# Performance work log

Measured on AMD Instinct MI355X. Metric: run time of the kernel, lower is better.

## Reference

```python
import jax, jax.numpy as jnp
import numpy as np
import math

COARSE_K = 20
FINE_K = 10
KNOWLEDGE_RANK = 128


def setup_inputs() -> dict:
    key = jax.random.key(0)
    ks = jax.random.split(key, 5)
    B, S, D = 2, 2048, 1024
    NK = 65536
    return {
        "x": jax.random.normal(ks[0], (B, S, D), dtype=jnp.float32),
        "W_router": jax.random.normal(ks[1], (D, NK), dtype=jnp.float32) * 0.02,
        "W_enc": jax.random.normal(ks[2], (D, KNOWLEDGE_RANK), dtype=jnp.float32) * 0.02,
        "K_all": jax.random.normal(ks[3], (NK, KNOWLEDGE_RANK), dtype=jnp.float32) * 0.02,
        "V_all": jax.random.normal(ks[4], (NK, D), dtype=jnp.float32) * 0.02,
    }


def reference(x, W_router, W_enc, K_all, V_all):
    # Stage 1: coarse routing over full knowledge table
    k_logits = jnp.einsum('bsd,dn->bsn', x, W_router)          # [B,S,NK]
    coarse_scores, candidate_idx = jax.lax.top_k(k_logits, COARSE_K)  # [B,S,Ck]

    # Stage 2: fine scoring against gathered coarse candidates
    query = jnp.einsum('bsd,dr->bsr', x, W_enc)                # [B,S,R]
    K_candidates = K_all[candidate_idx]                        # [B,S,Ck,R]
    fine_scores = jnp.einsum('bsr,bscr->bsc', query, K_candidates) / math.sqrt(KNOWLEDGE_RANK)

    fine_topk_scores, fine_local_idx = jax.lax.top_k(fine_scores, FINE_K)  # [B,S,Fk]
    fine_weights = jax.nn.softmax(fine_topk_scores, axis=-1)
    fine_global_idx = jnp.take_along_axis(candidate_idx, fine_local_idx, axis=-1)  # [B,S,Fk]

    selected_V = V_all[fine_global_idx]                        # [B,S,Fk,D]
    output = jnp.einsum('bsfd,bsf->bsd', selected_V, fine_weights)
    return output
```

## Files before the change

### kernel.cpp

```cpp
#include <hip/hip_runtime.h>

#define DIM 1024
#define NKN 65536
#define TOK 4096
#define CK 20
#define FK 10
#define RNK 128
#define CAP 256
#define NCHUNK 512

typedef __bf16 v8bf __attribute__((ext_vector_type(8)));
typedef float v4f __attribute__((ext_vector_type(4)));

#define AS1 __attribute__((address_space(1)))
#define AS3 __attribute__((address_space(3)))

__device__ __forceinline__ unsigned short f2bf(float f) {
  unsigned u = __builtin_bit_cast(unsigned, f);
  u += 0x7FFFu + ((u >> 16) & 1u);
  return (unsigned short)(u >> 16);
}
__device__ __forceinline__ unsigned short bf2key(unsigned short b) {
  return (b & 0x8000) ? (unsigned short)(~b) : (unsigned short)(b | 0x8000);
}

__global__ __launch_bounds__(256) void k_transpose(const float* __restrict__ W,
                                                   float* __restrict__ WT,
                                                   unsigned short* __restrict__ WTb) {
  __shared__ float tile[32][33];
  const int n0 = (blockIdx.x & 2047) << 5;
  const int d0 = (blockIdx.x >> 11) << 5;
  const int c = threadIdx.x & 31, r0 = threadIdx.x >> 5;
#pragma unroll
  for (int i = 0; i < 4; i++) {
    int r = r0 + i * 8;
    tile[r][c] = W[(size_t)(d0 + r) * NKN + n0 + c];
  }
  __syncthreads();
#pragma unroll
  for (int i = 0; i < 4; i++) {
    int r = r0 + i * 8;
    float v = tile[c][r];
    size_t o = (size_t)(n0 + r) * DIM + d0 + c;
    WT[o] = v;
    WTb[o] = f2bf(v);
  }
}

__global__ __launch_bounds__(256) void k_cvt_x(const float* __restrict__ x,
                                               unsigned short* __restrict__ xb) {
  const int i = blockIdx.x * 256 + threadIdx.x;
  const float4 v = reinterpret_cast<const float4*>(x)[i];
  ushort4 o;
  o.x = f2bf(v.x); o.y = f2bf(v.y); o.z = f2bf(v.z); o.w = f2bf(v.w);
  reinterpret_cast<ushort4*>(xb)[i] = o;
}

__global__ __launch_bounds__(512, 4) void k_gemm(const unsigned short* __restrict__ A,
                                                 const unsigned short* __restrict__ Bt,
                                                 unsigned short* __restrict__ Lg,
                                                 unsigned short* __restrict__ CmaxT) {
  __shared__ __align__(16) char lds[73728];
  const int tid = threadIdx.x;
  const int lane = tid & 63, wid = tid >> 6;
  const int wm = wid >> 1, wn = wid & 1;
  const int mb = blockIdx.x & 15, nb = blockIdx.x >> 4;
  const int m0 = mb << 8, n0 = nb << 7;
  const int rm = lane & 15, lq = lane >> 4;
  v4f acc[4][4] = {};

  const int u8 = (((tid & 3) ^ ((tid >> 3) & 3)) << 3);
  const unsigned short* aSrc = A + (size_t)(m0 + (tid >> 2)) * DIM + u8;
  const unsigned short* bSrc = Bt + (size_t)(n0 + (tid >> 2)) * DIM + u8;

  const int sx = ((lq ^ ((rm >> 1) & 3)) << 4);
  const int aOff = (wm * 64 + rm) * 64 + sx;
  const int bOff = 16384 + (wn * 64 + rm) * 64 + sx;

#define STAGE(SLOT, KT) do { \
    char* _b = lds + (SLOT) * 24576 + tid * 16; \
    __builtin_amdgcn_global_load_lds((const AS1 void*)(aSrc + (KT)),             (AS3 void*)(_b),         16, 0, 0); \
    __builtin_amdgcn_global_load_lds((const AS1 void*)(aSrc + (KT) + 128 * DIM), (AS3 void*)(_b + 8192),  16, 0, 0); \
    __builtin_amdgcn_global_load_lds((const AS1 void*)(bSrc + (KT)),             (AS3 void*)(_b + 16384), 16, 0, 0); \
  } while (0)

#define TILE(T, VM, DOSTAGE) do { \
    asm volatile("s_waitcnt vmcnt(" VM ")" ::: "memory"); \
    __builtin_amdgcn_s_barrier(); \
    if (DOSTAGE) STAGE(((T) + 2) % 3, ((T) + 2) * 32); \
    const char* sb = lds + ((T) % 3) * 24576; \
    v8bf a0 = *(const v8bf*)(sb + aOff); \
    v8bf a1 = *(const v8bf*)(sb + aOff + 1024); \
    v8bf a2 = *(const v8bf*)(sb + aOff + 2048); \
    v8bf a3 = *(const v8bf*)(sb + aOff + 3072); \
    v8bf b0 = *(const v8bf*)(sb + bOff); \
    v8bf b1 = *(const v8bf*)(sb + bOff + 1024); \
    v8bf b2 = *(const v8bf*)(sb + bOff + 2048); \
    v8bf b3 = *(const v8bf*)(sb + bOff + 3072); \
    __builtin_amdgcn_s_setprio(1); \
    _Pragma("unroll") for (int nf = 0; nf < 4; ++nf) { \
      v8bf bb = (nf == 0) ? b0 : (nf == 1) ? b1 : (nf == 2) ? b2 : b3; \
      acc[0][nf] = __builtin_amdgcn_mfma_f32_16x16x32_bf16(a0, bb, acc[0][nf], 0, 0, 0); \
      acc[1][nf] = __builtin_amdgcn_mfma_f32_16x16x32_bf16(a1, bb, acc[1][nf], 0, 0, 0); \
      acc[2][nf] = __builtin_amdgcn_mfma_f32_16x16x32_bf16(a2, bb, acc[2][nf], 0, 0, 0); \
      acc[3][nf] = __builtin_amdgcn_mfma_f32_16x16x32_bf16(a3, bb, acc[3][nf], 0, 0, 0); \
    } \
    __builtin_amdgcn_s_setprio(0); \
  } while (0)

  STAGE(0, 0);
  STAGE(1, 32);

  for (int t = 0; t < 30; ++t) {
    TILE(t, "3", true);
  }
  TILE(30, "3", false);
  TILE(31, "0", false);
#undef TILE
#undef STAGE

  const int mr = lq * 4;
  float rmax[4][4];
#pragma unroll
  for (int fr = 0; fr < 4; ++fr) {
#pragma unroll
    for (int r = 0; r < 4; ++r) {
      float mx = acc[fr][0][r];
#pragma unroll
      for (int nf = 1; nf < 4; ++nf) mx = fmaxf(mx, acc[fr][nf][r]);
      rmax[fr][r] = mx;
    }
#pragma unroll
    for (int nf = 0; nf < 4; ++nf) {
      const int mrow = m0 + wm * 64 + fr * 16 + mr;
      const int ncol = n0 + wn * 64 + nf * 16 + rm;
#pragma unroll
      for (int r = 0; r < 4; ++r)
        Lg[(size_t)(mrow + r) * NKN + ncol] = f2bf(acc[fr][nf][r]);
    }
  }
#pragma unroll
  for (int fr = 0; fr < 4; ++fr)
#pragma unroll
    for (int r = 0; r < 4; ++r) {
#pragma unroll
      for (int off = 1; off < 16; off <<= 1)
        rmax[fr][r] = fmaxf(rmax[fr][r], __shfl_xor(rmax[fr][r], off));
    }
  __syncthreads();
  float* smax = (float*)lds;
  if (rm == 0) {
#pragma unroll
    for (int fr = 0; fr < 4; ++fr)
#pragma unroll
      for (int r = 0; r < 4; ++r)
        smax[wn * 256 + wm * 64 + fr * 16 + mr + r] = rmax[fr][r];
  }
  __syncthreads();
  if (tid < 256) {
    float v = fmaxf(smax[tid], smax[256 + tid]);
    CmaxT[(size_t)nb * TOK + m0 + tid] = bf2key(f2bf(v));
  }
}

__global__ __launch_bounds__(256) void k_pickscore(const unsigned short* __restrict__ CmaxT,
                                                   const unsigned short* __restrict__ Lg,
                                                   const float* __restrict__ x,
                                                   const float* __restrict__ WT,
                                                   int* __restrict__ coarse) {
  __shared__ unsigned short keys[NCHUNK];
  __shared__ int qlist[NCHUNK];
  __shared__ float xs[DIM];
  __shared__ double sc[CAP];
  __shared__ int ci[CAP];
  __shared__ int qn, scnt, bsS;
  const int t = blockIdx.x, tid = threadIdx.x;
  const int lane = tid & 63, w = tid >> 6;
  keys[tid] = CmaxT[(size_t)tid * TOK + t];
  keys[tid + 256] = CmaxT[(size_t)(tid + 256) * TOK + t];
  for (int i = tid; i < DIM; i += 256) xs[i] = x[(size_t)t * DIM + i];
  if (tid == 0) { qn = 0; scnt = 0; }
  __syncthreads();
  if (w == 0) {
    int v[8];
#pragma unroll
    for (int j = 0; j < 8; j++) v[j] = keys[lane * 8 + j];
    int t32 = 0;
    for (int it = 0; it < 32; it++) {
      int lm = v[0];
#pragma unroll
      for (int j = 1; j < 8; j++) lm = max(lm, v[j]);
      int gm = lm;
#pragma unroll
      for (int off = 32; off > 0; off >>= 1) gm = max(gm, __shfl_xor(gm, off));
      unsigned long long msk = __ballot(lm == gm);
      if (lane == __ffsll((long long)msk) - 1) {
        bool done = false;
#pragma unroll
        for (int j = 0; j < 8; j++)
          if (!done && v[j] == gm) { v[j] = -1; done = true; }
      }
      t32 = gm;
    }
    if (lane == 0) bsS = t32;
  }
  __syncthreads();
  const int bs = bsS;
  for (int c = tid; c < NCHUNK; c += 256)
    if ((int)keys[c] >= bs) { int p = atomicAdd(&qn, 1); qlist[p] = c; }
  __syncthreads();
  const int nq = qn;
  const int sub = tid >> 7, e = tid & 127;
  for (int qi = sub; qi < nq; qi += 2) {
    const int col = qlist[qi] * 128 + e;
    unsigned short key = bf2key(Lg[(size_t)t * NKN + col]);
    if ((int)key >= bs) {
      int p = atomicAdd(&scnt, 1);
      if (p < CAP) ci[p] = col;
    }
  }
  __syncthreads();
  const int cnt = min(scnt, CAP);
  for (int i = tid; i < CAP; i += 256)
    if (i >= cnt) ci[i] = 0;
  for (int i = tid; i < CAP; i += 256) sc[i] = -1e300;
  __syncthreads();
  for (int c = w; c < cnt; c += 4) {
    const float* wr = WT + (size_t)ci[c] * DIM;
    double sacc = 0.0;
#pragma unroll 4
    for (int i = lane; i < DIM; i += 64) sacc += (double)xs[i] * (double)wr[i];
#pragma unroll
    for (int off = 32; off > 0; off >>= 1) sacc += __shfl_down(sacc, off);
    if (lane == 0) sc[c] = sacc;
  }
  __syncthreads();
  if (w == 0) {
    double v[4];
    int ix[4];
#pragma unroll
    for (int j = 0; j < 4; j++) { v[j] = sc[lane + j * 64]; ix[j] = lane + j * 64; }
    for (int kk = 0; kk < CK; kk++) {
      double v1 = v[0]; int i1 = ix[0];
#pragma unroll
      for (int j = 1; j < 4; j++)
        if (v[j] > v1) { v1 = v[j]; i1 = ix[j]; }
#pragma unroll
      for (int off = 32; off > 0; off >>= 1) {
        double ov = __shfl_down(v1, off);
        int oi = __shfl_down(i1, off);
        if (ov > v1) { v1 = ov; i1 = oi; }
      }
      i1 = __shfl(i1, 0);
      if (lane == 0) coarse[(size_t)t * CK + kk] = ci[i1];
#pragma unroll
      for (int j = 0; j < 4; j++)
        if (i1 == ix[j]) v[j] = -1e300;
    }
  }
}

__global__ __launch_bounds__(256) void k_fine(const float* __restrict__ x,
                                              const float* __restrict__ Wenc,
                                              const float* __restrict__ Kall,
                                              const float* __restrict__ Vall,
                                              const int* __restrict__ coarse,
                                              float* __restrict__ out) {
  __shared__ float xs[DIM];
  __shared__ float pq[2][RNK];
  __shared__ float qs[RNK];
  __shared__ float fsc[CK];
  __shared__ int gix[CK];
  __shared__ float wts[FK];
  __shared__ int fidx[FK];
  const int t = blockIdx.x, tid = threadIdx.x;
  const int lane = tid & 63, w = tid >> 6;
  reinterpret_cast<float4*>(xs)[tid] = reinterpret_cast<const float4*>(x + (size_t)t * DIM)[tid];
  if (tid < CK) gix[tid] = coarse[(size_t)t * CK + tid];
  __syncthreads();
  {
    const int j = tid & 127, half = tid >> 7;
    float s = 0.f;
    const int d0 = half * 512;
#pragma unroll 8
    for (int d = 0; d < 512; d++)
      s = fmaf(xs[d0 + d], Wenc[(size_t)(d0 + d) * RNK + j], s);
    pq[half][j] = s;
  }
  __syncthreads();
  if (tid < RNK) qs[tid] = pq[0][tid] + pq[1][tid];
  __syncthreads();
  for (int c = w; c < CK; c += 4) {
    const float* kr = Kall + (size_t)gix[c] * RNK;
    float s = 0.f;
    s = fmaf(qs[lane], kr[lane], s);
    s = fmaf(qs[lane + 64], kr[lane + 64], s);
#pragma unroll
    for (int off = 32; off > 0; off >>= 1) s += __shfl_down(s, off);
    if (lane == 0) fsc[c] = s * 0.08838834764831843f;
  }
  __syncthreads();
  if (w == 0) {
    float vv = (lane < CK) ? fsc[lane] : -3e38f;
    float myv = -3e38f; int myp = 0;
    for (int kk = 0; kk < FK; kk++) {
      float v1 = vv; int p1 = lane;
#pragma unroll
      for (int off = 32; off > 0; off >>= 1) {
        float ov = __shfl_down(v1, off);
        int op = __shfl_down(p1, off);
        if (ov > v1) { v1 = ov; p1 = op; }
      }
      v1 = __shfl(v1, 0); p1 = __shfl(p1, 0);
      if (lane == kk) { myv = v1; myp = p1; }
      if (lane == p1) vv = -3e38f;
    }
    float sv = (lane < FK) ? myv : -3e38f;
    float mx = sv;
#pragma unroll
    for (int off = 8; off > 0; off >>= 1) mx = fmaxf(mx, __shfl_xor(mx, off, 16));
    float e = (lane < FK) ? expf(sv - mx) : 0.f;
    float se = e;
#pragma unroll
    for (int off = 8; off > 0; off >>= 1) se += __shfl_xor(se, off, 16);
    if (lane < FK) { wts[lane] = e / se; fidx[lane] = gix[myp]; }
  }
  __syncthreads();
  float4 a = make_float4(0.f, 0.f, 0.f, 0.f);
#pragma unroll
  for (int f = 0; f < FK; f++) {
    const float wt = wts[f];
    const float4 v = *reinterpret_cast<const float4*>(&Vall[(size_t)fidx[f] * DIM + tid * 4]);
    a.x = fmaf(wt, v.x, a.x);
    a.y = fmaf(wt, v.y, a.y);
    a.z = fmaf(wt, v.z, a.z);
    a.w = fmaf(wt, v.w, a.w);
  }
  *reinterpret_cast<float4*>(&out[(size_t)t * DIM + tid * 4]) = a;
}


extern "C" void kernel_launch(void* const* d_in, const int* in_sizes, int n_in,
                              void* d_out, int out_size, void* d_ws, size_t ws_size,
                              hipStream_t stream) {
  const float* x = (const float*)d_in[0];
  const float* Wr = (const float*)d_in[1];
  const float* Wenc = (const float*)d_in[2];
  const float* Kall = (const float*)d_in[3];
  const float* Vall = (const float*)d_in[4];
  float* out = (float*)d_out;

  char* ws = (char*)d_ws;
  constexpr size_t OFF_WT = 0;
  constexpr size_t OFF_WTB = 268435456;
  constexpr size_t OFF_XB = 402653184;
  constexpr size_t OFF_LG = 411041792;
  constexpr size_t OFF_CMAX = 947912704;
  float* WT = (float*)(ws + OFF_WT);
  unsigned short* WTb = (unsigned short*)(ws + OFF_WTB);
  unsigned short* xb = (unsigned short*)(ws + OFF_XB);
  unsigned short* Lg = (unsigned short*)(ws + OFF_LG);
  unsigned short* CmaxT = (unsigned short*)(ws + OFF_CMAX);
  int* coarse = (int*)(ws + OFF_XB);

  k_transpose<<<65536, 256, 0, stream>>>(Wr, WT, WTb);
  k_cvt_x<<<4096, 256, 0, stream>>>(x, xb);
  k_gemm<<<8192, 512, 0, stream>>>(xb, WTb, Lg, CmaxT);
  k_pickscore<<<4096, 256, 0, stream>>>(CmaxT, Lg, x, WT, coarse);
  k_fine<<<4096, 256, 0, stream>>>(x, Wenc, Kall, Vall, coarse, out);
}
```

Baseline: 1.048 ms.

## Batch eight tokens per block in fine stage and widen pickscore blocks

k_fine now handles eight tokens per block, so each Wenc element it loads feeds eight query accumulators instead of one. This cuts the per-token reload of the 512KB Wenc matrix across 4096 blocks. k_pickscore moves to 512 threads with float4 loads for x and the rescoring dot products. The trade-off is fewer k_fine blocks (512), which lowers parallelism and raises register and LDS use per block.

```diff
diff --git a/kernel.cpp b/kernel.cpp
--- a/kernel.cpp
+++ b/kernel.cpp
@@ -163,22 +163,23 @@
   }
 }
 
-__global__ __launch_bounds__(256) void k_pickscore(const unsigned short* __restrict__ CmaxT,
+__global__ __launch_bounds__(512) void k_pickscore(const unsigned short* __restrict__ CmaxT,
                                                    const unsigned short* __restrict__ Lg,
                                                    const float* __restrict__ x,
                                                    const float* __restrict__ WT,
                                                    int* __restrict__ coarse) {
   __shared__ unsigned short keys[NCHUNK];
   __shared__ int qlist[NCHUNK];
-  __shared__ float xs[DIM];
+  __shared__ __align__(16) float xs[DIM];
   __shared__ double sc[CAP];
   __shared__ int ci[CAP];
   __shared__ int qn, scnt, bsS;
   const int t = blockIdx.x, tid = threadIdx.x;
   const int lane = tid & 63, w = tid >> 6;
   keys[tid] = CmaxT[(size_t)tid * TOK + t];
-  keys[tid + 256] = CmaxT[(size_t)(tid + 256) * TOK + t];
-  for (int i = tid; i < DIM; i += 256) xs[i] = x[(size_t)t * DIM + i];
+  if (tid < 256)
+    reinterpret_cast<float4*>(xs)[tid] =
+        reinterpret_cast<const float4*>(x + (size_t)t * DIM)[tid];
   if (tid == 0) { qn = 0; scnt = 0; }
   __syncthreads();
   if (w == 0) {
@@ -206,12 +207,11 @@
   }
   __syncthreads();
   const int bs = bsS;
-  for (int c = tid; c < NCHUNK; c += 256)
-    if ((int)keys[c] >= bs) { int p = atomicAdd(&qn, 1); qlist[p] = c; }
+  if ((int)keys[tid] >= bs) { int p = atomicAdd(&qn, 1); qlist[p] = tid; }
   __syncthreads();
   const int nq = qn;
   const int sub = tid >> 7, e = tid & 127;
-  for (int qi = sub; qi < nq; qi += 2) {
+  for (int qi = sub; qi < nq; qi += 4) {
     const int col = qlist[qi] * 128 + e;
     unsigned short key = bf2key(Lg[(size_t)t * NKN + col]);
     if ((int)key >= bs) {
@@ -221,15 +221,22 @@
   }
   __syncthreads();
   const int cnt = min(scnt, CAP);
-  for (int i = tid; i < CAP; i += 256)
+  for (int i = tid; i < CAP; i += 512) {
     if (i >= cnt) ci[i] = 0;
-  for (int i = tid; i < CAP; i += 256) sc[i] = -1e300;
-  __syncthreads();
-  for (int c = w; c < cnt; c += 4) {
-    const float* wr = WT + (size_t)ci[c] * DIM;
+    sc[i] = -1e300;
+  }
+  __syncthreads();
+  for (int c = w; c < cnt; c += 8) {
+    const float4* wr = reinterpret_cast<const float4*>(WT + (size_t)ci[c] * DIM);
+    const float4* xv4 = reinterpret_cast<const float4*>(xs);
     double sacc = 0.0;
-#pragma unroll 4
-    for (int i = lane; i < DIM; i += 64) sacc += (double)xs[i] * (double)wr[i];
+#pragma unroll
+    for (int k = 0; k < 4; k++) {
+      float4 wv = wr[k * 64 + lane];
+      float4 xv = xv4[k * 64 + lane];
+      sacc += (double)xv.x * wv.x + (double)xv.y * wv.y
+            + (double)xv.z * wv.z + (double)xv.w * wv.w;
+    }
 #pragma unroll
     for (int off = 32; off > 0; off >>= 1) sacc += __shfl_down(sacc, off);
     if (lane == 0) sc[c] = sacc;
@@ -266,42 +273,66 @@
                                               const float* __restrict__ Vall,
                                               const int* __restrict__ coarse,
                                               float* __restrict__ out) {
-  __shared__ float xs[DIM];
-  __shared__ float pq[2][RNK];
-  __shared__ float qs[RNK];
-  __shared__ float fsc[CK];
-  __shared__ int gix[CK];
-  __shared__ float wts[FK];
-  __shared__ int fidx[FK];
-  const int t = blockIdx.x, tid = threadIdx.x;
+  __shared__ __align__(16) float xs8[8][DIM];
+  __shared__ float pq[2][8][RNK];
+  __shared__ float q8[8][RNK];
+  __shared__ float fsc8[8][CK];
+  __shared__ int gix8[8][CK];
+  __shared__ float wts8[8][FK];
+  __shared__ int fidx8[8][FK];
+  const int t0 = blockIdx.x * 8, tid = threadIdx.x;
   const int lane = tid & 63, w = tid >> 6;
-  reinterpret_cast<float4*>(xs)[tid] = reinterpret_cast<const float4*>(x + (size_t)t * DIM)[tid];
-  if (tid < CK) gix[tid] = coarse[(size_t)t * CK + tid];
+  for (int i = tid; i < 2048; i += 256)
+    reinterpret_cast<float4*>(&xs8[0][0])[i] =
+        reinterpret_cast<const float4*>(x + (size_t)t0 * DIM)[i];
+  for (int i = tid; i < 8 * CK; i += 256)
+    gix8[i / CK][i % CK] = coarse[(size_t)(t0 + i / CK) * CK + i % CK];
   __syncthreads();
   {
-    const int j = tid & 127, half = tid >> 7;
-    float s = 0.f;
-    const int d0 = half * 512;
-#pragma unroll 8
-    for (int d = 0; d < 512; d++)
-      s = fmaf(xs[d0 + d], Wenc[(size_t)(d0 + d) * RNK + j], s);
-    pq[half][j] = s;
-  }
-  __syncthreads();
-  if (tid < RNK) qs[tid] = pq[0][tid] + pq[1][tid];
-  __syncthreads();
-  for (int c = w; c < CK; c += 4) {
-    const float* kr = Kall + (size_t)gix[c] * RNK;
-    float s = 0.f;
-    s = fmaf(qs[lane], kr[lane], s);
-    s = fmaf(qs[lane + 64], kr[lane + 64], s);
-#pragma unroll
-    for (int off = 32; off > 0; off >>= 1) s += __shfl_down(s, off);
-    if (lane == 0) fsc[c] = s * 0.08838834764831843f;
-  }
-  __syncthreads();
-  if (w == 0) {
-    float vv = (lane < CK) ? fsc[lane] : -3e38f;
+    const int j = tid & 127, g = tid >> 7;
+    float s[8] = {0.f, 0.f, 0.f, 0.f, 0.f, 0.f, 0.f, 0.f};
+    const float4* xv4 = reinterpret_cast<const float4*>(&xs8[0][0]);
+    for (int dc = g * 128; dc < g * 128 + 128; dc++) {
+      float4 xv[8];
+#pragma unroll
+      for (int tok = 0; tok < 8; tok++) xv[tok] = xv4[tok * 256 + dc];
+      const int d = dc * 4;
+      const float w0v = Wenc[(size_t)d * RNK + j];
+      const float w1v = Wenc[(size_t)(d + 1) * RNK + j];
+      const float w2v = Wenc[(size_t)(d + 2) * RNK + j];
+      const float w3v = Wenc[(size_t)(d + 3) * RNK + j];
+#pragma unroll
+      for (int tok = 0; tok < 8; tok++) {
+        s[tok] = fmaf(xv[tok].x, w0v, s[tok]);
+        s[tok] = fmaf(xv[tok].y, w1v, s[tok]);
+        s[tok] = fmaf(xv[tok].z, w2v, s[tok]);
+        s[tok] = fmaf(xv[tok].w, w3v, s[tok]);
+      }
+    }
+#pragma unroll
+    for (int tok = 0; tok < 8; tok++) pq[g][tok][j] = s[tok];
+  }
+  __syncthreads();
+  for (int i = tid; i < 8 * RNK; i += 256)
+    q8[i >> 7][i & 127] = pq[0][i >> 7][i & 127] + pq[1][i >> 7][i & 127];
+  __syncthreads();
+#pragma unroll
+  for (int tt = 0; tt < 2; tt++) {
+    const int tok = w + tt * 4;
+    for (int c = 0; c < CK; c++) {
+      const float* kr = Kall + (size_t)gix8[tok][c] * RNK;
+      float s = fmaf(q8[tok][lane], kr[lane], 0.f);
+      s = fmaf(q8[tok][lane + 64], kr[lane + 64], s);
+#pragma unroll
+      for (int off = 32; off > 0; off >>= 1) s += __shfl_down(s, off);
+      if (lane == 0) fsc8[tok][c] = s * 0.08838834764831843f;
+    }
+  }
+  __syncthreads();
+#pragma unroll
+  for (int tt = 0; tt < 2; tt++) {
+    const int tok = w + tt * 4;
+    float vv = (lane < CK) ? fsc8[tok][lane] : -3e38f;
     float myv = -3e38f; int myp = 0;
     for (int kk = 0; kk < FK; kk++) {
       float v1 = vv; int p1 = lane;
@@ -323,20 +354,23 @@
     float se = e;
 #pragma unroll
     for (int off = 8; off > 0; off >>= 1) se += __shfl_xor(se, off, 16);
-    if (lane < FK) { wts[lane] = e / se; fidx[lane] = gix[myp]; }
-  }
-  __syncthreads();
-  float4 a = make_float4(0.f, 0.f, 0.f, 0.f);
-#pragma unroll
-  for (int f = 0; f < FK; f++) {
-    const float wt = wts[f];
-    const float4 v = *reinterpret_cast<const float4*>(&Vall[(size_t)fidx[f] * DIM + tid * 4]);
-    a.x = fmaf(wt, v.x, a.x);
-    a.y = fmaf(wt, v.y, a.y);
-    a.z = fmaf(wt, v.z, a.z);
-    a.w = fmaf(wt, v.w, a.w);
-  }
-  *reinterpret_cast<float4*>(&out[(size_t)t * DIM + tid * 4]) = a;
+    if (lane < FK) { wts8[tok][lane] = e / se; fidx8[tok][lane] = gix8[tok][myp]; }
+  }
+  __syncthreads();
+  for (int tok = 0; tok < 8; tok++) {
+    float4 a = make_float4(0.f, 0.f, 0.f, 0.f);
+#pragma unroll
+    for (int f = 0; f < FK; f++) {
+      const float wt = wts8[tok][f];
+      const float4 v = *reinterpret_cast<const float4*>(
+          &Vall[(size_t)fidx8[tok][f] * DIM + tid * 4]);
+      a.x = fmaf(wt, v.x, a.x);
+      a.y = fmaf(wt, v.y, a.y);
+      a.z = fmaf(wt, v.z, a.z);
+      a.w = fmaf(wt, v.w, a.w);
+    }
+    *reinterpret_cast<float4*>(&out[(size_t)(t0 + tok) * DIM + tid * 4]) = a;
+  }
 }
 
 
@@ -366,6 +400,6 @@
   k_transpose<<<65536, 256, 0, stream>>>(Wr, WT, WTb);
   k_cvt_x<<<4096, 256, 0, stream>>>(x, xb);
   k_gemm<<<8192, 512, 0, stream>>>(xb, WTb, Lg, CmaxT);
-  k_pickscore<<<4096, 256, 0, stream>>>(CmaxT, Lg, x, WT, coarse);
-  k_fine<<<4096, 256, 0, stream>>>(x, Wenc, Kall, Vall, coarse, out);
-}
+  k_pickscore<<<4096, 512, 0, stream>>>(CmaxT, Lg, x, WT, coarse);
+  k_fine<<<512, 256, 0, stream>>>(x, Wenc, Kall, Vall, coarse, out);
+}
```

Result: slower. 1.104 ms (+5.3%).

## Emit per-chunk top-8 candidates from GEMM epilogue instead of full logits

Applied to the files above, without the earlier changes.

The GEMM epilogue stages bf16 sort keys for its 256x128 tile in LDS. Each row then keeps a sorted top-8 list of packed (key<<16 | column) values and writes only those eight words per row and chunk. This replaces the full bf16 logit matrix and the chunk-max array. The pickscore kernel reads these compact lists, derives the threshold from each chunk's best entry, and collects candidates directly without re-reading logits. The fp64 rescoring dot product also moves to float4 loads. This removes a very large global write and the later gather, at the cost of a serial insertion sort in the epilogue. It assumes no chunk holds more than eight of a row's threshold-passing entries.

```diff
diff --git a/kernel.cpp b/kernel.cpp
--- a/kernel.cpp
+++ b/kernel.cpp
@@ -58,8 +58,7 @@
 
 __global__ __launch_bounds__(512, 4) void k_gemm(const unsigned short* __restrict__ A,
                                                  const unsigned short* __restrict__ Bt,
-                                                 unsigned short* __restrict__ Lg,
-                                                 unsigned short* __restrict__ CmaxT) {
+                                                 unsigned* __restrict__ Ttop) {
   __shared__ __align__(16) char lds[73728];
   const int tid = threadIdx.x;
   const int lane = tid & 63, wid = tid >> 6;
@@ -119,72 +118,79 @@
 #undef TILE
 #undef STAGE
 
-  const int mr = lq * 4;
-  float rmax[4][4];
+  __syncthreads();
+  unsigned short* keys = (unsigned short*)lds;
 #pragma unroll
   for (int fr = 0; fr < 4; ++fr) {
-#pragma unroll
-    for (int r = 0; r < 4; ++r) {
-      float mx = acc[fr][0][r];
-#pragma unroll
-      for (int nf = 1; nf < 4; ++nf) mx = fmaxf(mx, acc[fr][nf][r]);
-      rmax[fr][r] = mx;
-    }
+    const int lrow = wm * 64 + fr * 16 + lq * 4;
 #pragma unroll
     for (int nf = 0; nf < 4; ++nf) {
-      const int mrow = m0 + wm * 64 + fr * 16 + mr;
-      const int ncol = n0 + wn * 64 + nf * 16 + rm;
+      const int lcol = wn * 64 + nf * 16 + rm;
 #pragma unroll
       for (int r = 0; r < 4; ++r)
-        Lg[(size_t)(mrow + r) * NKN + ncol] = f2bf(acc[fr][nf][r]);
-    }
-  }
-#pragma unroll
-  for (int fr = 0; fr < 4; ++fr)
-#pragma unroll
-    for (int r = 0; r < 4; ++r) {
-#pragma unroll
-      for (int off = 1; off < 16; off <<= 1)
-        rmax[fr][r] = fmaxf(rmax[fr][r], __shfl_xor(rmax[fr][r], off));
-    }
-  __syncthreads();
-  float* smax = (float*)lds;
-  if (rm == 0) {
-#pragma unroll
-    for (int fr = 0; fr < 4; ++fr)
-#pragma unroll
-      for (int r = 0; r < 4; ++r)
-        smax[wn * 256 + wm * 64 + fr * 16 + mr + r] = rmax[fr][r];
+        keys[(lrow + r) * 136 + lcol] = bf2key(f2bf(acc[fr][nf][r]));
+    }
   }
   __syncthreads();
   if (tid < 256) {
-    float v = fmaxf(smax[tid], smax[256 + tid]);
-    CmaxT[(size_t)nb * TOK + m0 + tid] = bf2key(f2bf(v));
-  }
-}
-
-__global__ __launch_bounds__(256) void k_pickscore(const unsigned short* __restrict__ CmaxT,
-                                                   const unsigned short* __restrict__ Lg,
+    const uint4* krow = (const uint4*)((const char*)lds + tid * 272);
+    unsigned s0 = 0, s1 = 0, s2 = 0, s3 = 0, s4 = 0, s5 = 0, s6 = 0, s7 = 0;
+#pragma unroll 4
+    for (int k = 0; k < 16; ++k) {
+      const uint4 wv = krow[k];
+      const unsigned base = (unsigned)(n0 + k * 8);
+      const unsigned wd[4] = {wv.x, wv.y, wv.z, wv.w};
+#pragma unroll
+      for (int q = 0; q < 4; ++q) {
+        const unsigned c0 = ((wd[q] & 0xFFFFu) << 16) | (base + 2 * q);
+        const unsigned c1 = (wd[q] & 0xFFFF0000u) | (base + 2 * q + 1);
+#define INS(C) \
+        if ((C) > s7) { \
+          s7 = (C); unsigned tswp; \
+          if (s7 > s6) { tswp = s6; s6 = s7; s7 = tswp; } \
+          if (s6 > s5) { tswp = s5; s5 = s6; s6 = tswp; } \
+          if (s5 > s4) { tswp = s4; s4 = s5; s5 = tswp; } \
+          if (s4 > s3) { tswp = s3; s3 = s4; s4 = tswp; } \
+          if (s3 > s2) { tswp = s2; s2 = s3; s3 = tswp; } \
+          if (s2 > s1) { tswp = s1; s1 = s2; s2 = tswp; } \
+          if (s1 > s0) { tswp = s0; s0 = s1; s1 = tswp; } \
+        }
+        INS(c0)
+        INS(c1)
+#undef INS
+      }
+    }
+    unsigned* dst = Ttop + ((size_t)(m0 + tid) * NCHUNK + nb) * 8;
+    uint4 o0 = {s0, s1, s2, s3}, o1 = {s4, s5, s6, s7};
+    reinterpret_cast<uint4*>(dst)[0] = o0;
+    reinterpret_cast<uint4*>(dst)[1] = o1;
+  }
+}
+
+__global__ __launch_bounds__(256) void k_pickscore(const unsigned* __restrict__ Ttop,
                                                    const float* __restrict__ x,
                                                    const float* __restrict__ WT,
                                                    int* __restrict__ coarse) {
-  __shared__ unsigned short keys[NCHUNK];
-  __shared__ int qlist[NCHUNK];
-  __shared__ float xs[DIM];
+  __shared__ unsigned ent[NCHUNK * 8];
+  __shared__ __align__(16) float xs[DIM];
   __shared__ double sc[CAP];
   __shared__ int ci[CAP];
-  __shared__ int qn, scnt, bsS;
+  __shared__ int scnt, bsS;
   const int t = blockIdx.x, tid = threadIdx.x;
   const int lane = tid & 63, w = tid >> 6;
-  keys[tid] = CmaxT[(size_t)tid * TOK + t];
-  keys[tid + 256] = CmaxT[(size_t)(tid + 256) * TOK + t];
-  for (int i = tid; i < DIM; i += 256) xs[i] = x[(size_t)t * DIM + i];
-  if (tid == 0) { qn = 0; scnt = 0; }
+  {
+    const uint4* src = reinterpret_cast<const uint4*>(Ttop + (size_t)t * NCHUNK * 8);
+    for (int i = tid; i < 1024; i += 256)
+      reinterpret_cast<uint4*>(ent)[i] = src[i];
+    reinterpret_cast<float4*>(xs)[tid] =
+        reinterpret_cast<const float4*>(x + (size_t)t * DIM)[tid];
+  }
+  if (tid == 0) scnt = 0;
   __syncthreads();
   if (w == 0) {
     int v[8];
 #pragma unroll
-    for (int j = 0; j < 8; j++) v[j] = keys[lane * 8 + j];
+    for (int j = 0; j < 8; j++) v[j] = (int)(ent[(lane * 8 + j) * 8] >> 16);
     int t32 = 0;
     for (int it = 0; it < 32; it++) {
       int lm = v[0];
@@ -205,31 +211,32 @@
     if (lane == 0) bsS = t32;
   }
   __syncthreads();
-  const int bs = bsS;
-  for (int c = tid; c < NCHUNK; c += 256)
-    if ((int)keys[c] >= bs) { int p = atomicAdd(&qn, 1); qlist[p] = c; }
-  __syncthreads();
-  const int nq = qn;
-  const int sub = tid >> 7, e = tid & 127;
-  for (int qi = sub; qi < nq; qi += 2) {
-    const int col = qlist[qi] * 128 + e;
-    unsigned short key = bf2key(Lg[(size_t)t * NKN + col]);
-    if ((int)key >= bs) {
+  const unsigned bs = (unsigned)bsS;
+  for (int i = tid; i < NCHUNK * 8; i += 256) {
+    const unsigned e = ent[i];
+    if ((e >> 16) >= bs) {
       int p = atomicAdd(&scnt, 1);
-      if (p < CAP) ci[p] = col;
+      if (p < CAP) ci[p] = (int)(e & 0xFFFFu);
     }
   }
   __syncthreads();
   const int cnt = min(scnt, CAP);
-  for (int i = tid; i < CAP; i += 256)
-    if (i >= cnt) ci[i] = 0;
-  for (int i = tid; i < CAP; i += 256) sc[i] = -1e300;
+  if (tid < CAP) {
+    if (tid >= cnt) ci[tid] = 0;
+    sc[tid] = -1e300;
+  }
   __syncthreads();
   for (int c = w; c < cnt; c += 4) {
-    const float* wr = WT + (size_t)ci[c] * DIM;
+    const float4* wr = reinterpret_cast<const float4*>(WT + (size_t)ci[c] * DIM);
+    const float4* xv4 = reinterpret_cast<const float4*>(xs);
     double sacc = 0.0;
-#pragma unroll 4
-    for (int i = lane; i < DIM; i += 64) sacc += (double)xs[i] * (double)wr[i];
+#pragma unroll
+    for (int k = 0; k < 4; k++) {
+      float4 wv = wr[k * 64 + lane];
+      float4 xv = xv4[k * 64 + lane];
+      sacc += (double)xv.x * wv.x + (double)xv.y * wv.y
+            + (double)xv.z * wv.z + (double)xv.w * wv.w;
+    }
 #pragma unroll
     for (int off = 32; off > 0; off >>= 1) sacc += __shfl_down(sacc, off);
     if (lane == 0) sc[c] = sacc;
@@ -354,18 +361,16 @@
   constexpr size_t OFF_WT = 0;
   constexpr size_t OFF_WTB = 268435456;
   constexpr size_t OFF_XB = 402653184;
-  constexpr size_t OFF_LG = 411041792;
-  constexpr size_t OFF_CMAX = 947912704;
+  constexpr size_t OFF_TTOP = 411041792;
   float* WT = (float*)(ws + OFF_WT);
   unsigned short* WTb = (unsigned short*)(ws + OFF_WTB);
   unsigned short* xb = (unsigned short*)(ws + OFF_XB);
-  unsigned short* Lg = (unsigned short*)(ws + OFF_LG);
-  unsigned short* CmaxT = (unsigned short*)(ws + OFF_CMAX);
+  unsigned* Ttop = (unsigned*)(ws + OFF_TTOP);
   int* coarse = (int*)(ws + OFF_XB);
 
   k_transpose<<<65536, 256, 0, stream>>>(Wr, WT, WTb);
   k_cvt_x<<<4096, 256, 0, stream>>>(x, xb);
-  k_gemm<<<8192, 512, 0, stream>>>(xb, WTb, Lg, CmaxT);
-  k_pickscore<<<4096, 256, 0, stream>>>(CmaxT, Lg, x, WT, coarse);
+  k_gemm<<<8192, 512, 0, stream>>>(xb, WTb, Ttop);
+  k_pickscore<<<4096, 256, 0, stream>>>(Ttop, x, WT, coarse);
   k_fine<<<4096, 256, 0, stream>>>(x, Wenc, Kall, Vall, coarse, out);
 }
```

Measured after the change: 985.9 us. 1.06x faster.
